# Optimization experiments

Measured on AMD Instinct MI355X. Metric: run time of the kernel, lower is better.

The kernel has to match this reference:

```python
import jax, jax.numpy as jnp
import numpy as np

MAX_DISP = 4  # matches init_kwargs


def setup_inputs() -> dict:
    key = jax.random.key(0)
    k1, k2 = jax.random.split(key)
    fmap1 = jax.random.normal(k1, (8, 256, 64, 128), dtype=jnp.float32)
    fmap2 = jax.random.normal(k2, (8, 256, 64, 128), dtype=jnp.float32)
    return {"fmap1": fmap1, "fmap2": fmap2}


def reference(fmap1, fmap2):
    # corr(x,y,dx,dy) = sum_c fmap1[c,y,x] * fmap2[c,y+dy,x+dx]
    pad = MAX_DISP
    B, C, H, W = fmap1.shape
    f2p = jnp.pad(fmap2, ((0, 0), (0, 0), (pad, pad), (pad, pad)))
    side = 2 * pad + 1  # 9 -> 81 displacements total
    # Loop over the small fixed set of 81 static displacements; each term is a
    # fused elementwise-multiply + channel reduction (einsum over c).
    corrs = [
        jnp.einsum('bchw,bchw->bhw', fmap1, f2p[:, :, y0:y0 + H, x0:x0 + W])
        for y0 in range(side)
        for x0 in range(side)
    ]
    return jnp.stack(corrs, axis=1)  # (B, 81, H, W)
```

## Files before the change

kernel.cpp:

```cpp
#include <hip/hip_runtime.h>


namespace {
constexpr int B_ = 8, C_ = 256, H_ = 64, W_ = 128;
constexpr int SIDE = 9, ND = 81, PAD = 4;
constexpr int HW = H_ * W_;
constexpr int KC = 32;
constexpr int NCH = C_ / KC;
constexpr int YB = 8;
constexpr int RWS = YB + 2 * PAD;
constexpr int XB = 16;
constexpr int F2PX = 32;
constexpr int PXS = KC / 2 + 4;
constexpr int F2U = RWS * (F2PX / 4) * (KC / 2);
constexpr int F1U = YB * (XB / 4) * (KC / 2);
}

typedef __attribute__((ext_vector_type(8))) short short8;
typedef __attribute__((ext_vector_type(4))) float float4v;

__device__ __forceinline__ unsigned bf16rne(float f) {
  unsigned u = __float_as_uint(f);
  return (u + 0x7fffu + ((u >> 16) & 1u)) >> 16;
}
__device__ __forceinline__ unsigned packbf2(float lo, float hi) {
  return bf16rne(lo) | (bf16rne(hi) << 16);
}

__global__ __launch_bounds__(512, 4)
void corr_fused(const float* __restrict__ f1, const float* __restrict__ f2,
                float* __restrict__ out) {
  __shared__ __align__(16) unsigned f2s[RWS * F2PX * PXS];
  __shared__ __align__(16) unsigned f1s[YB * XB * PXS];

  const int id = blockIdx.x;
  const int b = id & 7;
  const int k = id >> 3;
  const int xg = k & 7;
  const int yg = k >> 3;
  const int x0 = xg * XB;
  const int y0 = yg * YB;

  const int t = threadIdx.x;
  const int lane = t & 63;
  const int w = t >> 6;
  const int v = lane & 15;
  const int q = lane >> 4;

  float4v acc[SIDE][2];
#pragma unroll
  for (int i = 0; i < SIDE; ++i) {
    acc[i][0] = (float4v){0.f, 0.f, 0.f, 0.f};
    acc[i][1] = (float4v){0.f, 0.f, 0.f, 0.f};
  }

  const float* __restrict__ f1b = f1 + (size_t)b * C_ * HW;
  const float* __restrict__ f2b = f2 + (size_t)b * C_ * HW;

  for (int ch = 0; ch < NCH; ++ch) {
    const int c0 = ch * KC;
    if (ch) __syncthreads();

#pragma unroll
    for (int u0 = 0; u0 < F2U; u0 += 512) {
      const int u = u0 + t;
      const int cp = u & 15;
      const int t2 = u >> 4;
      const int pxq = t2 & 7;
      const int r = t2 >> 3;
      const int ygl = y0 - PAD + r;
      const int xb = x0 - PAD + pxq * 4;
      float4 va = make_float4(0.f, 0.f, 0.f, 0.f), vb = va;
      if (ygl >= 0 && ygl < H_ && xb >= 0 && xb <= W_ - 4) {
        const float* p = f2b + ((size_t)(c0 + 2 * cp) * H_ + ygl) * W_ + xb;
        va = *(const float4*)p;
        vb = *(const float4*)(p + HW);
      }
      unsigned* d = &f2s[(r * F2PX + pxq * 4) * PXS + cp];
      d[0 * PXS] = packbf2(va.x, vb.x);
      d[1 * PXS] = packbf2(va.y, vb.y);
      d[2 * PXS] = packbf2(va.z, vb.z);
      d[3 * PXS] = packbf2(va.w, vb.w);
    }
    {
      const int cp = t & 15;
      const int t2 = t >> 4;
      const int pxq = t2 & 3;
      const int r = t2 >> 2;
      const float* p =
          f1b + ((size_t)(c0 + 2 * cp) * H_ + (y0 + r)) * W_ + x0 + pxq * 4;
      const float4 va = *(const float4*)p;
      const float4 vb = *(const float4*)(p + HW);
      unsigned* d = &f1s[(r * XB + pxq * 4) * PXS + cp];
      d[0 * PXS] = packbf2(va.x, vb.x);
      d[1 * PXS] = packbf2(va.y, vb.y);
      d[2 * PXS] = packbf2(va.z, vb.z);
      d[3 * PXS] = packbf2(va.w, vb.w);
    }
    __syncthreads();

    const short8 af = __builtin_bit_cast(
        short8, *(const uint4*)&f1s[(w * XB + v) * PXS + 4 * q]);
#pragma unroll
    for (int dy = 0; dy < SIDE; ++dy) {
      const unsigned* fp = &f2s[((w + dy) * F2PX + v) * PXS + 4 * q];
      const short8 b0 = __builtin_bit_cast(short8, *(const uint4*)fp);
      const short8 b1 =
          __builtin_bit_cast(short8, *(const uint4*)(fp + 16 * PXS));
      acc[dy][0] =
          __builtin_amdgcn_mfma_f32_16x16x32_bf16(af, b0, acc[dy][0], 0, 0, 0);
      acc[dy][1] =
          __builtin_amdgcn_mfma_f32_16x16x32_bf16(af, b1, acc[dy][1], 0, 0, 0);
    }
  }

  const int y = y0 + w;
  float* outb = out + (size_t)b * ND * HW + (size_t)y * W_ + x0;
#pragma unroll
  for (int dy = 0; dy < SIDE; ++dy) {
#pragma unroll
    for (int r = 0; r < 4; ++r) {
      const int m = q * 4 + r;
      const int dx0 = v - m;
      if (dx0 >= 0 && dx0 <= 8)
        outb[(size_t)(dy * SIDE + dx0) * HW + m] = acc[dy][0][r];
      const int dx1 = v - m + 16;
      if (dx1 <= 8)
        outb[(size_t)(dy * SIDE + dx1) * HW + m] = acc[dy][1][r];
    }
  }
}

extern "C" void kernel_launch(void* const* d_in, const int* in_sizes, int n_in,
                              void* d_out, int out_size, void* d_ws,
                              size_t ws_size, hipStream_t stream) {
  (void)in_sizes; (void)n_in; (void)out_size; (void)d_ws; (void)ws_size;
  const float* f1 = (const float*)d_in[0];
  const float* f2 = (const float*)d_in[1];
  float* out = (float*)d_out;
  corr_fused<<<dim3(512), 512, 0, stream>>>(f1, f2, out);
}
```

Before: 178.8 us.

## Prefetch next channel chunk into registers and load fmap1 fragments directly

Loads of fmap2 for the next channel chunk are issued into registers before the MFMA loop of the current chunk, so global memory latency overlaps with compute. fmap1 is now read straight into per-lane registers in the MFMA A-operand layout, which removes the fmap1 shared-memory tile and its LDS round-trip. Launch bounds drop to 2 blocks per SM to make room for the extra prefetch registers, which may reduce occupancy. The fmap1 loads become scalar strided accesses rather than float4.

```diff
diff --git a/kernel.cpp b/kernel.cpp
--- a/kernel.cpp
+++ b/kernel.cpp
@@ -12,8 +12,6 @@
 constexpr int XB = 16;
 constexpr int F2PX = 32;
 constexpr int PXS = KC / 2 + 4;
-constexpr int F2U = RWS * (F2PX / 4) * (KC / 2);
-constexpr int F1U = YB * (XB / 4) * (KC / 2);
 }
 
 typedef __attribute__((ext_vector_type(8))) short short8;
@@ -27,11 +25,10 @@
   return bf16rne(lo) | (bf16rne(hi) << 16);
 }
 
-__global__ __launch_bounds__(512, 4)
+__global__ __launch_bounds__(512, 2)
 void corr_fused(const float* __restrict__ f1, const float* __restrict__ f2,
                 float* __restrict__ out) {
   __shared__ __align__(16) unsigned f2s[RWS * F2PX * PXS];
-  __shared__ __align__(16) unsigned f1s[YB * XB * PXS];
 
   const int id = blockIdx.x;
   const int b = id & 7;
@@ -47,6 +44,38 @@
   const int v = lane & 15;
   const int q = lane >> 4;
 
+  const int cp2 = t & 15;
+  const int pxq2 = (t >> 4) & 7;
+  const int r0 = t >> 7;
+  const int xb = x0 - PAD + pxq2 * 4;
+  const bool xok = (xb >= 0 && xb <= W_ - 4);
+
+  const float* __restrict__ f1b = f1 + (size_t)b * C_ * HW;
+  const float* __restrict__ f2b = f2 + (size_t)b * C_ * HW;
+
+  float4 pa[4], pb[4];
+  float pf1[8];
+
+  auto loadf2 = [&](int c0) {
+#pragma unroll
+    for (int i = 0; i < 4; ++i) {
+      const int ygl = y0 - PAD + r0 + 4 * i;
+      float4 va = make_float4(0.f, 0.f, 0.f, 0.f), vb = va;
+      if (xok && ygl >= 0 && ygl < H_) {
+        const float* p = f2b + ((size_t)(c0 + 2 * cp2) * H_ + ygl) * W_ + xb;
+        va = *(const float4*)p;
+        vb = *(const float4*)(p + HW);
+      }
+      pa[i] = va;
+      pb[i] = vb;
+    }
+  };
+  auto loadf1 = [&](int c0) {
+    const float* p = f1b + ((size_t)(c0 + 8 * q) * H_ + (y0 + w)) * W_ + x0 + v;
+#pragma unroll
+    for (int j = 0; j < 8; ++j) pf1[j] = p[(size_t)j * HW];
+  };
+
   float4v acc[SIDE][2];
 #pragma unroll
   for (int i = 0; i < SIDE; ++i) {
@@ -54,53 +83,38 @@
     acc[i][1] = (float4v){0.f, 0.f, 0.f, 0.f};
   }
 
-  const float* __restrict__ f1b = f1 + (size_t)b * C_ * HW;
-  const float* __restrict__ f2b = f2 + (size_t)b * C_ * HW;
+  loadf2(0);
+  loadf1(0);
 
+#pragma unroll
   for (int ch = 0; ch < NCH; ++ch) {
-    const int c0 = ch * KC;
     if (ch) __syncthreads();
 
+    {
+      unsigned* d0 = &f2s[(size_t)(pxq2 * 4) * PXS + cp2];
 #pragma unroll
-    for (int u0 = 0; u0 < F2U; u0 += 512) {
-      const int u = u0 + t;
-      const int cp = u & 15;
-      const int t2 = u >> 4;
-      const int pxq = t2 & 7;
-      const int r = t2 >> 3;
-      const int ygl = y0 - PAD + r;
-      const int xb = x0 - PAD + pxq * 4;
-      float4 va = make_float4(0.f, 0.f, 0.f, 0.f), vb = va;
-      if (ygl >= 0 && ygl < H_ && xb >= 0 && xb <= W_ - 4) {
-        const float* p = f2b + ((size_t)(c0 + 2 * cp) * H_ + ygl) * W_ + xb;
-        va = *(const float4*)p;
-        vb = *(const float4*)(p + HW);
+      for (int i = 0; i < 4; ++i) {
+        unsigned* d = d0 + (size_t)(r0 + 4 * i) * F2PX * PXS;
+        d[0 * PXS] = packbf2(pa[i].x, pb[i].x);
+        d[1 * PXS] = packbf2(pa[i].y, pb[i].y);
+        d[2 * PXS] = packbf2(pa[i].z, pb[i].z);
+        d[3 * PXS] = packbf2(pa[i].w, pb[i].w);
       }
-      unsigned* d = &f2s[(r * F2PX + pxq * 4) * PXS + cp];
-      d[0 * PXS] = packbf2(va.x, vb.x);
-      d[1 * PXS] = packbf2(va.y, vb.y);
-      d[2 * PXS] = packbf2(va.z, vb.z);
-      d[3 * PXS] = packbf2(va.w, vb.w);
     }
-    {
-      const int cp = t & 15;
-      const int t2 = t >> 4;
-      const int pxq = t2 & 3;
-      const int r = t2 >> 2;
-      const float* p =
-          f1b + ((size_t)(c0 + 2 * cp) * H_ + (y0 + r)) * W_ + x0 + pxq * 4;
-      const float4 va = *(const float4*)p;
-      const float4 vb = *(const float4*)(p + HW);
-      unsigned* d = &f1s[(r * XB + pxq * 4) * PXS + cp];
-      d[0 * PXS] = packbf2(va.x, vb.x);
-      d[1 * PXS] = packbf2(va.y, vb.y);
-      d[2 * PXS] = packbf2(va.z, vb.z);
-      d[3 * PXS] = packbf2(va.w, vb.w);
-    }
+    uint4 afu;
+    afu.x = packbf2(pf1[0], pf1[1]);
+    afu.y = packbf2(pf1[2], pf1[3]);
+    afu.z = packbf2(pf1[4], pf1[5]);
+    afu.w = packbf2(pf1[6], pf1[7]);
+    const short8 af = __builtin_bit_cast(short8, afu);
+
     __syncthreads();
 
-    const short8 af = __builtin_bit_cast(
-        short8, *(const uint4*)&f1s[(w * XB + v) * PXS + 4 * q]);
+    if (ch + 1 < NCH) {
+      loadf2((ch + 1) * KC);
+      loadf1((ch + 1) * KC);
+    }
+
 #pragma unroll
     for (int dy = 0; dy < SIDE; ++dy) {
       const unsigned* fp = &f2s[((w + dy) * F2PX + v) * PXS + 4 * q];
```

Result: slower. 184.1 us (+3.0%).

## Pre-convert fmap2 to padded bf16 layout and double-buffer it via direct LDS loads

Applied to the files above, without the earlier changes.

Adds a prepass kernel that converts fmap2 into a zero-padded, channel-interleaved bf16 workspace. The main kernel then streams tiles of that workspace into LDS with global_load_lds, double-buffered and with XOR swizzling. fmap1 for the next chunk is prefetched into registers while the current chunk's MFMAs run. This is meant to remove the per-block redundant fp32 loads and bf16 packing of the overlapping fmap2 halo, and to hide load latency behind compute. The cost is an extra kernel launch plus a workspace write and read. If the workspace is too small, the code falls back to the original kernel.

```diff
diff --git a/kernel.cpp b/kernel.cpp
--- a/kernel.cpp
+++ b/kernel.cpp
@@ -5,19 +5,23 @@
 constexpr int B_ = 8, C_ = 256, H_ = 64, W_ = 128;
 constexpr int SIDE = 9, ND = 81, PAD = 4;
 constexpr int HW = H_ * W_;
-constexpr int KC = 32;
-constexpr int NCH = C_ / KC;
-constexpr int YB = 8;
-constexpr int RWS = YB + 2 * PAD;
+constexpr int KC = 32, NCH = C_ / KC;
+constexpr int YB = 8, RWS = YB + 2 * PAD;
 constexpr int XB = 16;
-constexpr int F2PX = 32;
-constexpr int PXS = KC / 2 + 4;
-constexpr int F2U = RWS * (F2PX / 4) * (KC / 2);
-constexpr int F1U = YB * (XB / 4) * (KC / 2);
+constexpr int NQ = 4;
+constexpr int YP_ = H_ + 2 * PAD;
+constexpr int XP_ = 144;
+constexpr size_t ROWU = (size_t)NQ * XP_;
+constexpr size_t PERB = (size_t)NCH * YP_ * ROWU;
+constexpr size_t NW2 = (size_t)B_ * PERB;
+constexpr size_t WS_BYTES = NW2 * 16;
+constexpr int TILE_U4 = RWS * NQ * 32;
 }
 
 typedef __attribute__((ext_vector_type(8))) short short8;
 typedef __attribute__((ext_vector_type(4))) float float4v;
+typedef __attribute__((address_space(1))) void gvoid;
+typedef __attribute__((address_space(3))) void svoid;
 
 __device__ __forceinline__ unsigned bf16rne(float f) {
   unsigned u = __float_as_uint(f);
@@ -27,25 +31,68 @@
   return bf16rne(lo) | (bf16rne(hi) << 16);
 }
 
+__global__ __launch_bounds__(256)
+void cvt_f2(const float* __restrict__ f2, uint4* __restrict__ w2) {
+  const int id = blockIdx.x;
+  const int b = id & 7;
+  const int e = (id >> 3) * 256 + (int)threadIdx.x;
+  const int xp = e % XP_;
+  int r = e / XP_;
+  const int q = r & 3;
+  r >>= 2;
+  const int yp = r % YP_;
+  const int cs = r / YP_;
+  const int yg = yp - PAD, xg = xp - PAD;
+  uint4 o = {0u, 0u, 0u, 0u};
+  if (yg >= 0 && yg < H_ && xg >= 0 && xg < W_) {
+    const float* s = f2 + ((size_t)(b * C_ + cs * KC + q * 8) * H_ + yg) * W_ + xg;
+    o.x = packbf2(s[0 * HW], s[1 * HW]);
+    o.y = packbf2(s[2 * HW], s[3 * HW]);
+    o.z = packbf2(s[4 * HW], s[5 * HW]);
+    o.w = packbf2(s[6 * HW], s[7 * HW]);
+  }
+  w2[(size_t)b * PERB + e] = o;
+}
+
 __global__ __launch_bounds__(512, 4)
-void corr_fused(const float* __restrict__ f1, const float* __restrict__ f2,
+void corr_mfma2(const float* __restrict__ f1, const uint4* __restrict__ w2,
                 float* __restrict__ out) {
-  __shared__ __align__(16) unsigned f2s[RWS * F2PX * PXS];
-  __shared__ __align__(16) unsigned f1s[YB * XB * PXS];
+  __shared__ uint4 f2s[2 * TILE_U4];
 
   const int id = blockIdx.x;
   const int b = id & 7;
   const int k = id >> 3;
-  const int xg = k & 7;
-  const int yg = k >> 3;
-  const int x0 = xg * XB;
-  const int y0 = yg * YB;
-
-  const int t = threadIdx.x;
-  const int lane = t & 63;
-  const int w = t >> 6;
-  const int v = lane & 15;
-  const int q = lane >> 4;
+  const int xg = k & 7, yg = k >> 3;
+  const int x0 = xg * XB, y0 = yg * YB;
+
+  const int t = threadIdx.x, lane = t & 63, w = t >> 6;
+  const int v = lane & 15, q = lane >> 4;
+  const int sq = q << 1;
+  const int l_hi = lane >> 5;
+  const int l_xq = lane & 31;
+
+  const uint4* w2b = w2 + (size_t)b * PERB;
+  const float* f1b = f1 + (size_t)b * C_ * HW;
+
+  auto issue_stage = [&](int ch, int buf) {
+    const uint4* wc = w2b + (size_t)ch * ((size_t)YP_ * ROWU);
+#pragma unroll
+    for (int kk = 0; kk < 4; ++kk) {
+      const int r = 2 * w + (kk >> 1);
+      const int qp = kk & 1;
+      const int qq = 2 * qp + l_hi;
+      const int xqs = l_xq ^ (qq << 1);
+      const uint4* gp = wc + (size_t)(y0 + r) * ROWU + (size_t)qq * XP_ + x0 + xqs;
+      uint4* lp = &f2s[buf * TILE_U4 + (r * NQ + qp * 2) * 32];
+      __builtin_amdgcn_global_load_lds((gvoid*)gp, (svoid*)lp, 16, 0, 0);
+    }
+  };
+  auto issue_f1 = [&](int ch, float* p) {
+    const float* fp =
+        f1b + ((size_t)(ch * KC + q * 8) * H_ + (y0 + w)) * W_ + x0 + v;
+#pragma unroll
+    for (int j = 0; j < 8; ++j) p[j] = fp[(size_t)j * HW];
+  };
 
   float4v acc[SIDE][2];
 #pragma unroll
@@ -54,13 +101,95 @@
     acc[i][1] = (float4v){0.f, 0.f, 0.f, 0.f};
   }
 
+  float p0[8], p1[8];
+  issue_stage(0, 0);
+  __builtin_amdgcn_sched_barrier(0);
+  issue_f1(0, p0);
+  __builtin_amdgcn_sched_barrier(0);
+  issue_stage(1, 1);
+  __builtin_amdgcn_sched_barrier(0);
+
+#pragma unroll
+  for (int ch = 0; ch < NCH; ++ch) {
+    float* pc = (ch & 1) ? p1 : p0;
+    uint4 afu;
+    afu.x = packbf2(pc[0], pc[1]);
+    afu.y = packbf2(pc[2], pc[3]);
+    afu.z = packbf2(pc[4], pc[5]);
+    afu.w = packbf2(pc[6], pc[7]);
+    const short8 af = __builtin_bit_cast(short8, afu);
+
+    asm volatile("s_waitcnt vmcnt(4)" ::: "memory");
+    __builtin_amdgcn_s_barrier();
+    __builtin_amdgcn_sched_barrier(0);
+
+    if (ch + 1 < NCH) issue_f1(ch + 1, (ch & 1) ? p0 : p1);
+
+    const int bo = (ch & 1) * TILE_U4;
+#pragma unroll
+    for (int dy = 0; dy < SIDE; ++dy) {
+      const uint4* base = &f2s[bo + ((w + dy) * NQ + q) * 32];
+      const short8 b0 = __builtin_bit_cast(short8, base[v ^ sq]);
+      const short8 b1 = __builtin_bit_cast(short8, base[(v + 16) ^ sq]);
+      acc[dy][0] =
+          __builtin_amdgcn_mfma_f32_16x16x32_bf16(af, b0, acc[dy][0], 0, 0, 0);
+      acc[dy][1] =
+          __builtin_amdgcn_mfma_f32_16x16x32_bf16(af, b1, acc[dy][1], 0, 0, 0);
+    }
+    __builtin_amdgcn_sched_barrier(0);
+    __builtin_amdgcn_s_barrier();
+    __builtin_amdgcn_sched_barrier(0);
+    if (ch + 2 < NCH) issue_stage(ch + 2, ch & 1);
+  }
+
+  const int y = y0 + w;
+  float* outb = out + (size_t)b * ND * HW + (size_t)y * W_ + x0;
+#pragma unroll
+  for (int dy = 0; dy < SIDE; ++dy) {
+#pragma unroll
+    for (int r = 0; r < 4; ++r) {
+      const int m = q * 4 + r;
+      const int dx0 = v - m;
+      if (dx0 >= 0 && dx0 <= 8)
+        outb[(size_t)(dy * SIDE + dx0) * HW + m] = acc[dy][0][r];
+      const int dx1 = v - m + 16;
+      if (dx1 <= 8)
+        outb[(size_t)(dy * SIDE + dx1) * HW + m] = acc[dy][1][r];
+    }
+  }
+}
+
+namespace fb {
+constexpr int PXS = 20, F2PX = 32, F2U = 16 * (F2PX / 4) * 16;
+}
+
+__global__ __launch_bounds__(512, 4)
+void corr_fb(const float* __restrict__ f1, const float* __restrict__ f2,
+             float* __restrict__ out) {
+  using namespace fb;
+  __shared__ __align__(16) unsigned f2s[RWS * F2PX * PXS];
+  __shared__ __align__(16) unsigned f1s[YB * XB * PXS];
+
+  const int id = blockIdx.x;
+  const int b = id & 7;
+  const int k = id >> 3;
+  const int xg = k & 7, yg = k >> 3;
+  const int x0 = xg * XB, y0 = yg * YB;
+  const int t = threadIdx.x, lane = t & 63, w = t >> 6;
+  const int v = lane & 15, q = lane >> 4;
+
+  float4v acc[SIDE][2];
+#pragma unroll
+  for (int i = 0; i < SIDE; ++i) {
+    acc[i][0] = (float4v){0.f, 0.f, 0.f, 0.f};
+    acc[i][1] = (float4v){0.f, 0.f, 0.f, 0.f};
+  }
   const float* __restrict__ f1b = f1 + (size_t)b * C_ * HW;
   const float* __restrict__ f2b = f2 + (size_t)b * C_ * HW;
 
   for (int ch = 0; ch < NCH; ++ch) {
     const int c0 = ch * KC;
     if (ch) __syncthreads();
-
 #pragma unroll
     for (int u0 = 0; u0 < F2U; u0 += 512) {
       const int u = u0 + t;
@@ -113,7 +242,6 @@
           __builtin_amdgcn_mfma_f32_16x16x32_bf16(af, b1, acc[dy][1], 0, 0, 0);
     }
   }
-
   const int y = y0 + w;
   float* outb = out + (size_t)b * ND * HW + (size_t)y * W_ + x0;
 #pragma unroll
@@ -134,9 +262,15 @@
 extern "C" void kernel_launch(void* const* d_in, const int* in_sizes, int n_in,
                               void* d_out, int out_size, void* d_ws,
                               size_t ws_size, hipStream_t stream) {
-  (void)in_sizes; (void)n_in; (void)out_size; (void)d_ws; (void)ws_size;
+  (void)in_sizes; (void)n_in; (void)out_size;
   const float* f1 = (const float*)d_in[0];
   const float* f2 = (const float*)d_in[1];
   float* out = (float*)d_out;
-  corr_fused<<<dim3(512), 512, 0, stream>>>(f1, f2, out);
-}
+  if (ws_size >= WS_BYTES) {
+    uint4* w2 = (uint4*)d_ws;
+    cvt_f2<<<dim3((unsigned)(NW2 / 256)), 256, 0, stream>>>(f2, w2);
+    corr_mfma2<<<dim3(512), 512, 0, stream>>>(f1, w2, out);
+  } else {
+    corr_fb<<<dim3(512), 512, 0, stream>>>(f1, f2, out);
+  }
+}
```

Measured after the change: 182.6 us. 1.02x slower.
